# Performance work log

Measured on AMD Instinct MI355X. Metric: run time of the kernel, lower is better.

## Reference

```python
import jax, jax.numpy as jnp
import numpy as np

N_NODES = 100000


def gcn_conv(x, edge_index, W, b):
    """GCNConv: out = D^-1/2 (A + I) D^-1/2 (x W) + b, with added self-loops."""
    n = x.shape[0]
    xw = x @ W  # [N, C]
    loop = jnp.arange(n, dtype=edge_index.dtype)
    src = jnp.concatenate([edge_index[0], loop])  # [E+N]
    dst = jnp.concatenate([edge_index[1], loop])
    deg = jax.ops.segment_sum(jnp.ones_like(dst, dtype=xw.dtype), dst, num_segments=n)
    dinv = jax.lax.rsqrt(jnp.where(deg > 0, deg, 1.0))
    norm = dinv[src] * dinv[dst]  # [E+N]
    msgs = xw[src] * norm[:, None]  # gather + scale
    out = jax.ops.segment_sum(msgs, dst, num_segments=n)  # scatter-add
    return out + b


def setup_inputs() -> dict:
    key = jax.random.key(0)
    k1, k2, k3, k4, k5 = jax.random.split(key, 5)
    F_in, C1, C2 = 256, 64, 40
    E = 3200000
    x = jax.random.normal(k1, (N_NODES, F_in), dtype=jnp.float32)
    edge_index = jax.random.randint(k2, (2, E), 0, N_NODES, dtype=jnp.int64)
    W1 = jax.random.normal(k3, (F_in, C1), dtype=jnp.float32) / np.sqrt(F_in)
    b1 = jnp.zeros((C1,), dtype=jnp.float32)
    W2 = jax.random.normal(k4, (C1, C2), dtype=jnp.float32) / np.sqrt(C1)
    b2 = jnp.zeros((C2,), dtype=jnp.float32)
    return {"x": x, "edge_index": edge_index, "W1": W1, "b1": b1, "W2": W2, "b2": b2}


def reference(x, edge_index, W1, b1, W2, b2):
    h1 = jax.nn.relu(gcn_conv(x, edge_index, W1, b1))
    # dropout is identity in eval mode (training=False)
    h2 = gcn_conv(h1, edge_index, W2, b2)
    return jax.nn.log_softmax(h2, axis=1)
```

## Files before the change

kernel.cpp:

```cpp
#include <hip/hip_runtime.h>
#include <math.h>

#define NN 100000
#define NB 256
#define RANGE 392
#define CAP 56
#define BCAP 13824
#define NBLK_PART 512

typedef unsigned int uint;
typedef __attribute__((ext_vector_type(8))) short short8;
typedef __attribute__((ext_vector_type(4))) float f32x4;


__global__ __launch_bounds__(256) void partition_kernel(const int* __restrict__ src,
                                                        const int* __restrict__ dst,
                                                        int* __restrict__ bcur,
                                                        unsigned* __restrict__ bkt, int E) {
    __shared__ unsigned stage[NB * CAP];
    __shared__ int lcnt[NB];
    __shared__ int baseS[NB];
    for (int i = threadIdx.x; i < NB; i += 256) lcnt[i] = 0;
    __syncthreads();

    const int nq = E >> 2;
    const int stride = gridDim.x * blockDim.x;
    for (int q = blockIdx.x * blockDim.x + threadIdx.x; q < nq; q += stride) {
        const int4 s4 = ((const int4*)src)[q];
        const int4 d4 = ((const int4*)dst)[q];
#pragma unroll
        for (int k = 0; k < 4; k++) {
            const int s = (&s4.x)[k];
            const int d = (&d4.x)[k];
            const unsigned b = (unsigned)d / RANGE;
            const unsigned ent = ((unsigned)s << 9) | ((unsigned)d - b * RANGE);
            const int slot = atomicAdd(&lcnt[b], 1);
            if (slot < CAP) {
                stage[b * CAP + slot] = ent;
            } else {
                const int pos = atomicAdd(&bcur[b], 1);
                if (pos < BCAP) bkt[(size_t)b * BCAP + pos] = ent;
            }
        }
    }
    const int gid = blockIdx.x * blockDim.x + threadIdx.x;
    if (gid < (E & 3)) {
        const int e = (E & ~3) + gid;
        const int s = src[e], d = dst[e];
        const unsigned b = (unsigned)d / RANGE;
        const unsigned ent = ((unsigned)s << 9) | ((unsigned)d - b * RANGE);
        const int pos = atomicAdd(&bcur[b], 1);
        if (pos < BCAP) bkt[(size_t)b * BCAP + pos] = ent;
    }
    __syncthreads();

    if (threadIdx.x < NB) {
        const int c = min(lcnt[threadIdx.x], CAP);
        baseS[threadIdx.x] = (c > 0) ? atomicAdd(&bcur[threadIdx.x], c) : 0;
    }
    __syncthreads();

    const int w = threadIdx.x >> 6, l = threadIdx.x & 63;
    for (int b = w; b < NB; b += 4) {
        const int cnt = min(lcnt[b], CAP);
        const int base = baseS[b];
        for (int i = l; i < cnt; i += 64) {
            const int pos = base + i;
            if (pos < BCAP) bkt[(size_t)b * BCAP + pos] = stage[b * CAP + i];
        }
    }
}


__global__ __launch_bounds__(256) void bucket_sort_kernel(const int* __restrict__ bcur,
                                                          unsigned* __restrict__ bkt,
                                                          int* __restrict__ row_off,
                                                          int* __restrict__ deg,
                                                          float* __restrict__ dinv, int n) {
    __shared__ int sortedS[BCAP];
    __shared__ int cntS[RANGE];
    __shared__ int offS[RANGE];
    const int b = blockIdx.x;
    const int tid = threadIdx.x;
    unsigned* eb = bkt + (size_t)b * BCAP;
    const int m = min(bcur[b], BCAP);

    for (int i = tid; i < RANGE; i += 256) cntS[i] = 0;
    __syncthreads();
    for (int i = tid; i < m; i += 256) atomicAdd(&cntS[(int)(eb[i] & 511u)], 1);
    __syncthreads();

    if (tid < 64) {
        const int l = tid;
        int carry = 0;
        for (int base = 0; base < RANGE; base += 64) {
            const int i = base + l;
            const int c = (i < RANGE) ? cntS[i] : 0;
            int v = c;
#pragma unroll
            for (int off = 1; off < 64; off <<= 1) {
                const int t2 = __shfl_up(v, off);
                if (l >= off) v += t2;
            }
            if (i < RANGE) offS[i] = carry + v - c;
            carry += __shfl(v, 63);
        }
    }
    __syncthreads();

    for (int i = tid; i < RANGE; i += 256) {
        const int node = b * RANGE + i;
        if (node < n) {
            row_off[node] = b * BCAP + offS[i];
            deg[node] = cntS[i];
            dinv[node] = rsqrtf((float)cntS[i] + 1.0f);
        }
    }
    __syncthreads();

    for (int i = tid; i < m; i += 256) {
        const unsigned e = eb[i];
        const int pos = atomicAdd(&offS[(int)(e & 511u)], 1);
        sortedS[pos] = (int)(e >> 9);
    }
    __syncthreads();

    for (int i = tid; i < m; i += 256) eb[i] = (unsigned)sortedS[i];
}

__device__ inline uint pack_bf16(float a, float b) {
    uint ua = __float_as_uint(a), ub = __float_as_uint(b);
    ua = (ua + 0x7fffu + ((ua >> 16) & 1u)) >> 16;
    ub = (ub + 0x7fffu + ((ub >> 16) & 1u)) & 0xffff0000u;
    return ua | ub;
}
__device__ inline unsigned short bf16r(float f) {
    uint u = __float_as_uint(f);
    return (unsigned short)((u + 0x7fffu + ((u >> 16) & 1u)) >> 16);
}
__device__ inline void acc_bf16x8(float* acc, uint4 v) {
    const uint u[4] = {v.x, v.y, v.z, v.w};
#pragma unroll
    for (int i = 0; i < 4; i++) {
        acc[2 * i]     += __uint_as_float(u[i] << 16);
        acc[2 * i + 1] += __uint_as_float(u[i] & 0xffff0000u);
    }
}


template <int K, int CREAL>
__global__ __launch_bounds__(256) void gemm_mfma_kernel(const float* __restrict__ x,
                                                        const float* __restrict__ W,
                                                        const float* __restrict__ dinv,
                                                        unsigned short* __restrict__ y,
                                                        int n) {
    constexpr int KP = K + 8;
    __shared__ unsigned short wt[64 * KP];
    __shared__ unsigned short as[128 * 40];
    const int t = threadIdx.x;
    const int l = t & 63;
    const int w = t >> 6;
    const int lane15 = l & 15;
    const int quad = l >> 4;
    const int row0 = blockIdx.x * 128;

    for (int idx = t; idx < K * 16; idx += 256) {
        const int k = idx >> 4;
        const int c4 = (idx & 15) * 4;
        float4 g = make_float4(0.f, 0.f, 0.f, 0.f);
        if (c4 < CREAL) g = *(const float4*)(W + (size_t)k * CREAL + c4);
        wt[(c4 + 0) * KP + k] = bf16r(g.x);
        wt[(c4 + 1) * KP + k] = bf16r(g.y);
        wt[(c4 + 2) * KP + k] = bf16r(g.z);
        wt[(c4 + 3) * KP + k] = bf16r(g.w);
    }

    f32x4 acc[2][4];
#pragma unroll
    for (int mt = 0; mt < 2; mt++)
#pragma unroll
        for (int nt = 0; nt < 4; nt++) acc[mt][nt] = (f32x4){0.f, 0.f, 0.f, 0.f};

    float4 g[4];
#pragma unroll
    for (int p = 0; p < 4; p++) {
        const int idx = t + p * 256;
        const int row = idx >> 3;
        const int kq = idx & 7;
        const int gr = min(row0 + row, n - 1);
        g[p] = *(const float4*)(x + (size_t)gr * K + kq * 4);
    }

    for (int kc = 0; kc < K; kc += 32) {
        __syncthreads();
#pragma unroll
        for (int p = 0; p < 4; p++) {
            const int idx = t + p * 256;
            const int row = idx >> 3;
            const int kq = idx & 7;
            uint2 pk;
            pk.x = pack_bf16(g[p].x, g[p].y);
            pk.y = pack_bf16(g[p].z, g[p].w);
            *(uint2*)(as + row * 40 + kq * 4) = pk;
        }
        if (kc + 32 < K) {
#pragma unroll
            for (int p = 0; p < 4; p++) {
                const int idx = t + p * 256;
                const int row = idx >> 3;
                const int kq = idx & 7;
                const int gr = min(row0 + row, n - 1);
                g[p] = *(const float4*)(x + (size_t)gr * K + kc + 32 + kq * 4);
            }
        }
        __syncthreads();

        short8 bf[4];
#pragma unroll
        for (int nt = 0; nt < 4; nt++)
            bf[nt] = *(const short8*)(wt + (nt * 16 + lane15) * KP + kc + quad * 8);
#pragma unroll
        for (int mt = 0; mt < 2; mt++) {
            const short8 af =
                *(const short8*)(as + (w * 32 + mt * 16 + lane15) * 40 + quad * 8);
#pragma unroll
            for (int nt = 0; nt < 4; nt++)
                acc[mt][nt] =
                    __builtin_amdgcn_mfma_f32_16x16x32_bf16(af, bf[nt], acc[mt][nt], 0, 0, 0);
        }
    }

#pragma unroll
    for (int mt = 0; mt < 2; mt++) {
#pragma unroll
        for (int r = 0; r < 4; r++) {
            const int row = row0 + w * 32 + mt * 16 + quad * 4 + r;
            if (row < n) {
                const float di = dinv[row];
#pragma unroll
                for (int nt = 0; nt < 4; nt++)
                    y[(size_t)row * 64 + nt * 16 + lane15] = bf16r(acc[mt][nt][r] * di);
            }
        }
    }
}


__global__ __launch_bounds__(256) void agg64_kernel(const unsigned short* __restrict__ y,
                                                    const int* __restrict__ row_off,
                                                    const int* __restrict__ deg,
                                                    const unsigned* __restrict__ nbr,
                                                    const float* __restrict__ dinv,
                                                    const float* __restrict__ b,
                                                    float* __restrict__ out, int n) {
    int node = blockIdx.x * 4 + (threadIdx.x >> 6);
    if (node >= n) return;
    const int l = threadIdx.x & 63;
    const int g = l >> 3;
    const int cq = l & 7;

    const int start = row_off[node];
    const int dg = deg[node];

    float acc[8];
#pragma unroll
    for (int i = 0; i < 8; i++) acc[i] = 0.f;

    for (int base = 0; base < dg; base += 64) {
        const int m = min(64, dg - base);
        const int idx = (l < m) ? (int)nbr[start + base + l] : 0;
        for (int j0 = 0; j0 < m; j0 += 16) {
            const int jA = j0 + g;
            const int jB = j0 + 8 + g;
            const int sA = __shfl(idx, jA);
            const int sB = __shfl(idx, jB);
            const bool okA = jA < m;
            const bool okB = jB < m;
            uint4 vA = ((const uint4*)(y + (size_t)sA * 64))[cq];
            uint4 vB = ((const uint4*)(y + (size_t)sB * 64))[cq];
            vA.x = okA ? vA.x : 0u; vA.y = okA ? vA.y : 0u;
            vA.z = okA ? vA.z : 0u; vA.w = okA ? vA.w : 0u;
            vB.x = okB ? vB.x : 0u; vB.y = okB ? vB.y : 0u;
            vB.z = okB ? vB.z : 0u; vB.w = okB ? vB.w : 0u;
            acc_bf16x8(acc, vA);
            acc_bf16x8(acc, vB);
        }
    }
#pragma unroll
    for (int off = 8; off < 64; off <<= 1)
#pragma unroll
        for (int i = 0; i < 8; i++) acc[i] += __shfl_xor(acc[i], off);

    float self[8];
#pragma unroll
    for (int i = 0; i < 8; i++) self[i] = 0.f;
    acc_bf16x8(self, ((const uint4*)(y + (size_t)node * 64))[cq]);
    const float di = dinv[node];
    const float4 bv0 = *(const float4*)(b + cq * 8);
    const float4 bv1 = *(const float4*)(b + cq * 8 + 4);
    const float bb[8] = {bv0.x, bv0.y, bv0.z, bv0.w, bv1.x, bv1.y, bv1.z, bv1.w};
    if (l < 8) {
        float4 o0, o1;
        o0.x = fmaxf((acc[0] + self[0]) * di + bb[0], 0.f);
        o0.y = fmaxf((acc[1] + self[1]) * di + bb[1], 0.f);
        o0.z = fmaxf((acc[2] + self[2]) * di + bb[2], 0.f);
        o0.w = fmaxf((acc[3] + self[3]) * di + bb[3], 0.f);
        o1.x = fmaxf((acc[4] + self[4]) * di + bb[4], 0.f);
        o1.y = fmaxf((acc[5] + self[5]) * di + bb[5], 0.f);
        o1.z = fmaxf((acc[6] + self[6]) * di + bb[6], 0.f);
        o1.w = fmaxf((acc[7] + self[7]) * di + bb[7], 0.f);
        *(float4*)(out + (size_t)node * 64 + l * 8) = o0;
        *(float4*)(out + (size_t)node * 64 + l * 8 + 4) = o1;
    }
}


__global__ __launch_bounds__(256) void agg40_lsm_kernel(const unsigned short* __restrict__ y,
                                                        const int* __restrict__ row_off,
                                                        const int* __restrict__ deg,
                                                        const unsigned* __restrict__ nbr,
                                                        const float* __restrict__ dinv,
                                                        const float* __restrict__ b,
                                                        float* __restrict__ out, int n) {
    int node = blockIdx.x * 4 + (threadIdx.x >> 6);
    if (node >= n) return;
    const int l = threadIdx.x & 63;
    const int g = l >> 3;
    const int cq = l & 7;
    const bool real = (cq < 5);

    const int start = row_off[node];
    const int dg = deg[node];

    float acc[8];
#pragma unroll
    for (int i = 0; i < 8; i++) acc[i] = 0.f;

    for (int base = 0; base < dg; base += 64) {
        const int m = min(64, dg - base);
        const int idx = (l < m) ? (int)nbr[start + base + l] : 0;
        for (int j0 = 0; j0 < m; j0 += 16) {
            const int jA = j0 + g;
            const int jB = j0 + 8 + g;
            const int sA = __shfl(idx, jA);
            const int sB = __shfl(idx, jB);
            const bool okA = jA < m;
            const bool okB = jB < m;
            uint4 vA = ((const uint4*)(y + (size_t)sA * 64))[cq];
            uint4 vB = ((const uint4*)(y + (size_t)sB * 64))[cq];
            vA.x = okA ? vA.x : 0u; vA.y = okA ? vA.y : 0u;
            vA.z = okA ? vA.z : 0u; vA.w = okA ? vA.w : 0u;
            vB.x = okB ? vB.x : 0u; vB.y = okB ? vB.y : 0u;
            vB.z = okB ? vB.z : 0u; vB.w = okB ? vB.w : 0u;
            acc_bf16x8(acc, vA);
            acc_bf16x8(acc, vB);
        }
    }
#pragma unroll
    for (int off = 8; off < 64; off <<= 1)
#pragma unroll
        for (int i = 0; i < 8; i++) acc[i] += __shfl_xor(acc[i], off);

    float self[8];
#pragma unroll
    for (int i = 0; i < 8; i++) self[i] = 0.f;
    acc_bf16x8(self, ((const uint4*)(y + (size_t)node * 64))[cq]);
    const float di = dinv[node];
    float bb[8];
#pragma unroll
    for (int i = 0; i < 8; i++) bb[i] = 0.f;
    if (real) {
        const float4 bv0 = *(const float4*)(b + cq * 8);
        const float4 bv1 = *(const float4*)(b + cq * 8 + 4);
        bb[0] = bv0.x; bb[1] = bv0.y; bb[2] = bv0.z; bb[3] = bv0.w;
        bb[4] = bv1.x; bb[5] = bv1.y; bb[6] = bv1.z; bb[7] = bv1.w;
    }
    float h[8];
#pragma unroll
    for (int i = 0; i < 8; i++) h[i] = (acc[i] + self[i]) * di + bb[i];

    float mx = -INFINITY;
    if (real)
#pragma unroll
        for (int i = 0; i < 8; i++) mx = fmaxf(mx, h[i]);
#pragma unroll
    for (int off = 1; off < 8; off <<= 1) mx = fmaxf(mx, __shfl_xor(mx, off));
    float es = 0.f;
    if (real)
#pragma unroll
        for (int i = 0; i < 8; i++) es += __expf(h[i] - mx);
#pragma unroll
    for (int off = 1; off < 8; off <<= 1) es += __shfl_xor(es, off);
    const float ls = mx + __logf(es);

    if (l < 5) {
        float4 o0, o1;
        o0.x = h[0] - ls; o0.y = h[1] - ls; o0.z = h[2] - ls; o0.w = h[3] - ls;
        o1.x = h[4] - ls; o1.y = h[5] - ls; o1.z = h[6] - ls; o1.w = h[7] - ls;
        *(float4*)(out + (size_t)node * 40 + l * 8) = o0;
        *(float4*)(out + (size_t)node * 40 + l * 8 + 4) = o1;
    }
}


extern "C" void kernel_launch(void* const* d_in, const int* in_sizes, int n_in,
                              void* d_out, int out_size, void* d_ws, size_t ws_size,
                              hipStream_t stream) {
    const float* x  = (const float*)d_in[0];
    const int* edges = (const int*)d_in[1];
    const float* W1 = (const float*)d_in[2];
    const float* b1 = (const float*)d_in[3];
    const float* W2 = (const float*)d_in[4];
    const float* b2 = (const float*)d_in[5];
    float* out = (float*)d_out;

    const int n = NN;
    const int E = in_sizes[1] / 2;

    char* ws = (char*)d_ws;
    size_t off = 0;
    auto alloc = [&](size_t bytes) -> void* {
        void* p = ws + off;
        off += (bytes + 255) & ~(size_t)255;
        return p;
    };
    int*            bcur    = (int*)alloc((size_t)NB * 4);
    unsigned*       bkt     = (unsigned*)alloc((size_t)NB * BCAP * 4);
    int*            row_off = (int*)alloc((size_t)n * 4);
    int*            deg     = (int*)alloc((size_t)n * 4);
    float*          dinv    = (float*)alloc((size_t)n * 4);
    float*          h1      = (float*)alloc((size_t)n * 64 * 4);
    unsigned short* y1      = (unsigned short*)alloc((size_t)n * 64 * 2);
    unsigned short* y2      = y1;

    const int* src = edges;
    const int* dst = edges + E;

    hipMemsetAsync(bcur, 0, (size_t)NB * 4, stream);
    partition_kernel<<<NBLK_PART, 256, 0, stream>>>(src, dst, bcur, bkt, E);
    bucket_sort_kernel<<<NB, 256, 0, stream>>>(bcur, bkt, row_off, deg, dinv, n);

    const int gblk = (n + 127) / 128;

    gemm_mfma_kernel<256, 64><<<gblk, 256, 0, stream>>>(x, W1, dinv, y1, n);
    agg64_kernel<<<(n + 3) / 4, 256, 0, stream>>>(y1, row_off, deg, bkt, dinv, b1, h1, n);

    gemm_mfma_kernel<64, 40><<<gblk, 256, 0, stream>>>(h1, W2, dinv, y2, n);
    agg40_lsm_kernel<<<(n + 3) / 4, 256, 0, stream>>>(y2, row_off, deg, bkt, dinv, b2, out, n);
}
```

Baseline: 366.4 us.

## Store layer-2 features densely at 40 columns and use a zero sentinel row

The GEMM now writes y with stride CREAL instead of 64 and zeroes an extra sentinel row at index n. Both aggregation kernels point out-of-range neighbor slots at that zero row, which removes the per-element masking. The 40-channel aggregation is remapped to 5 channel-quads × 12 edge groups across the wave, cutting gathered bytes per edge from 128 to 80 and wasting fewer lanes. In exchange the reductions become uneven shfl_down trees with cross-group broadcasts for the softmax, and 4 lanes per wave do redundant work.

```diff
diff --git a/kernel.cpp b/kernel.cpp
--- a/kernel.cpp
+++ b/kernel.cpp
@@ -164,6 +164,8 @@
     const int quad = l >> 4;
     const int row0 = blockIdx.x * 128;
 
+    if (blockIdx.x == 0 && t < CREAL) y[(size_t)n * CREAL + t] = 0;
+
     for (int idx = t; idx < K * 16; idx += 256) {
         const int k = idx >> 4;
         const int c4 = (idx & 15) * 4;
@@ -238,8 +240,11 @@
             if (row < n) {
                 const float di = dinv[row];
 #pragma unroll
-                for (int nt = 0; nt < 4; nt++)
-                    y[(size_t)row * 64 + nt * 16 + lane15] = bf16r(acc[mt][nt][r] * di);
+                for (int nt = 0; nt < 4; nt++) {
+                    const int col = nt * 16 + lane15;
+                    if (col < CREAL)
+                        y[(size_t)row * CREAL + col] = bf16r(acc[mt][nt][r] * di);
+                }
             }
         }
     }
@@ -268,20 +273,12 @@
 
     for (int base = 0; base < dg; base += 64) {
         const int m = min(64, dg - base);
-        const int idx = (l < m) ? (int)nbr[start + base + l] : 0;
+        const int idx = (l < m) ? (int)nbr[start + base + l] : n;
         for (int j0 = 0; j0 < m; j0 += 16) {
-            const int jA = j0 + g;
-            const int jB = j0 + 8 + g;
-            const int sA = __shfl(idx, jA);
-            const int sB = __shfl(idx, jB);
-            const bool okA = jA < m;
-            const bool okB = jB < m;
-            uint4 vA = ((const uint4*)(y + (size_t)sA * 64))[cq];
-            uint4 vB = ((const uint4*)(y + (size_t)sB * 64))[cq];
-            vA.x = okA ? vA.x : 0u; vA.y = okA ? vA.y : 0u;
-            vA.z = okA ? vA.z : 0u; vA.w = okA ? vA.w : 0u;
-            vB.x = okB ? vB.x : 0u; vB.y = okB ? vB.y : 0u;
-            vB.z = okB ? vB.z : 0u; vB.w = okB ? vB.w : 0u;
+            const int sA = __shfl(idx, j0 + g);
+            const int sB = __shfl(idx, j0 + 8 + g);
+            const uint4 vA = ((const uint4*)(y + (size_t)sA * 64))[cq];
+            const uint4 vB = ((const uint4*)(y + (size_t)sB * 64))[cq];
             acc_bf16x8(acc, vA);
             acc_bf16x8(acc, vB);
         }
@@ -325,9 +322,10 @@
     int node = blockIdx.x * 4 + (threadIdx.x >> 6);
     if (node >= n) return;
     const int l = threadIdx.x & 63;
-    const int g = l >> 3;
-    const int cq = l & 7;
-    const bool real = (cq < 5);
+    const int cq0 = l / 12;
+    const int g = l - cq0 * 12;
+    const int cq = min(cq0, 4);
+    const bool lead = (g == 0) && (cq0 < 5);
 
     const int start = row_off[node];
     const int dg = deg[node];
@@ -336,69 +334,62 @@
 #pragma unroll
     for (int i = 0; i < 8; i++) acc[i] = 0.f;
 
-    for (int base = 0; base < dg; base += 64) {
-        const int m = min(64, dg - base);
-        const int idx = (l < m) ? (int)nbr[start + base + l] : 0;
-        for (int j0 = 0; j0 < m; j0 += 16) {
-            const int jA = j0 + g;
-            const int jB = j0 + 8 + g;
-            const int sA = __shfl(idx, jA);
-            const int sB = __shfl(idx, jB);
-            const bool okA = jA < m;
-            const bool okB = jB < m;
-            uint4 vA = ((const uint4*)(y + (size_t)sA * 64))[cq];
-            uint4 vB = ((const uint4*)(y + (size_t)sB * 64))[cq];
-            vA.x = okA ? vA.x : 0u; vA.y = okA ? vA.y : 0u;
-            vA.z = okA ? vA.z : 0u; vA.w = okA ? vA.w : 0u;
-            vB.x = okB ? vB.x : 0u; vB.y = okB ? vB.y : 0u;
-            vB.z = okB ? vB.z : 0u; vB.w = okB ? vB.w : 0u;
-            acc_bf16x8(acc, vA);
-            acc_bf16x8(acc, vB);
-        }
-    }
-#pragma unroll
-    for (int off = 8; off < 64; off <<= 1)
-#pragma unroll
-        for (int i = 0; i < 8; i++) acc[i] += __shfl_xor(acc[i], off);
-
-    float self[8];
-#pragma unroll
-    for (int i = 0; i < 8; i++) self[i] = 0.f;
-    acc_bf16x8(self, ((const uint4*)(y + (size_t)node * 64))[cq]);
+    for (int base = 0; base < dg; base += 60) {
+        const int m = min(60, dg - base);
+        const int idx = (l < m) ? (int)nbr[start + base + l] : n;
+        for (int r = 0; r * 12 < m; ++r) {
+            const int s = __shfl(idx, r * 12 + g);
+            const uint4 v = *((const uint4*)(y + (size_t)s * 40) + cq);
+            acc_bf16x8(acc, v);
+        }
+    }
+
+#pragma unroll
+    for (int i = 0; i < 8; i++) { const float t = __shfl_down(acc[i], 8); if (g < 4) acc[i] += t; }
+#pragma unroll
+    for (int i = 0; i < 8; i++) { const float t = __shfl_down(acc[i], 4); if (g < 4) acc[i] += t; }
+#pragma unroll
+    for (int i = 0; i < 8; i++) { const float t = __shfl_down(acc[i], 2); if (g < 2) acc[i] += t; }
+#pragma unroll
+    for (int i = 0; i < 8; i++) { const float t = __shfl_down(acc[i], 1); if (g == 0) acc[i] += t; }
+
+    if (lead) {
+        const uint4 v = *((const uint4*)(y + (size_t)node * 40) + cq);
+        acc_bf16x8(acc, v);
+    }
+
     const float di = dinv[node];
-    float bb[8];
-#pragma unroll
-    for (int i = 0; i < 8; i++) bb[i] = 0.f;
-    if (real) {
-        const float4 bv0 = *(const float4*)(b + cq * 8);
-        const float4 bv1 = *(const float4*)(b + cq * 8 + 4);
-        bb[0] = bv0.x; bb[1] = bv0.y; bb[2] = bv0.z; bb[3] = bv0.w;
-        bb[4] = bv1.x; bb[5] = bv1.y; bb[6] = bv1.z; bb[7] = bv1.w;
-    }
+    const float4 bv0 = *(const float4*)(b + cq * 8);
+    const float4 bv1 = *(const float4*)(b + cq * 8 + 4);
+    const float bb[8] = {bv0.x, bv0.y, bv0.z, bv0.w, bv1.x, bv1.y, bv1.z, bv1.w};
     float h[8];
 #pragma unroll
-    for (int i = 0; i < 8; i++) h[i] = (acc[i] + self[i]) * di + bb[i];
+    for (int i = 0; i < 8; i++) h[i] = acc[i] * di + bb[i];
 
     float mx = -INFINITY;
-    if (real)
-#pragma unroll
-        for (int i = 0; i < 8; i++) mx = fmaxf(mx, h[i]);
-#pragma unroll
-    for (int off = 1; off < 8; off <<= 1) mx = fmaxf(mx, __shfl_xor(mx, off));
+#pragma unroll
+    for (int i = 0; i < 8; i++) mx = fmaxf(mx, h[i]);
+    {
+        const float m0 = __shfl(mx, 0), m1 = __shfl(mx, 12), m2 = __shfl(mx, 24),
+                    m3 = __shfl(mx, 36), m4 = __shfl(mx, 48);
+        mx = fmaxf(fmaxf(fmaxf(m0, m1), fmaxf(m2, m3)), m4);
+    }
     float es = 0.f;
-    if (real)
-#pragma unroll
-        for (int i = 0; i < 8; i++) es += __expf(h[i] - mx);
-#pragma unroll
-    for (int off = 1; off < 8; off <<= 1) es += __shfl_xor(es, off);
+#pragma unroll
+    for (int i = 0; i < 8; i++) es += __expf(h[i] - mx);
+    {
+        const float e0 = __shfl(es, 0), e1 = __shfl(es, 12), e2 = __shfl(es, 24),
+                    e3 = __shfl(es, 36), e4 = __shfl(es, 48);
+        es = ((e0 + e1) + (e2 + e3)) + e4;
+    }
     const float ls = mx + __logf(es);
 
-    if (l < 5) {
+    if (lead) {
         float4 o0, o1;
         o0.x = h[0] - ls; o0.y = h[1] - ls; o0.z = h[2] - ls; o0.w = h[3] - ls;
         o1.x = h[4] - ls; o1.y = h[5] - ls; o1.z = h[6] - ls; o1.w = h[7] - ls;
-        *(float4*)(out + (size_t)node * 40 + l * 8) = o0;
-        *(float4*)(out + (size_t)node * 40 + l * 8 + 4) = o1;
+        *(float4*)(out + (size_t)node * 40 + cq * 8) = o0;
+        *(float4*)(out + (size_t)node * 40 + cq * 8 + 4) = o1;
     }
 }
 
@@ -430,7 +421,7 @@
     int*            deg     = (int*)alloc((size_t)n * 4);
     float*          dinv    = (float*)alloc((size_t)n * 4);
     float*          h1      = (float*)alloc((size_t)n * 64 * 4);
-    unsigned short* y1      = (unsigned short*)alloc((size_t)n * 64 * 2);
+    unsigned short* y1      = (unsigned short*)alloc((size_t)(n + 1) * 64 * 2);
     unsigned short* y2      = y1;
 
     const int* src = edges;
```

Measured after the change: 371.1 us. No clear change (+1.3%).
